# Kernel tuning notes

Hardware: AMD Instinct MI355X
Metric: run time of the kernel (lower is better)

## Reference

```python
import jax, jax.numpy as jnp
import numpy as np

C = 256; G = 16; GC = C // G; K = 3; P = K * K
N = 4; H = 64; W = 64
PAD = 1; OFFSET_SCALE = 1.0; LN_EPS = 1e-5


def setup_inputs() -> dict:
    key = jax.random.key(0)
    ks = jax.random.split(key, 8)
    s = 0.02
    return {
        "x": jax.random.normal(ks[0], (N, C, H, W), jnp.float32),
        "dw_w": jax.random.normal(ks[1], (C, 1, K, K), jnp.float32) * s,
        "dw_b": jnp.zeros((C,), jnp.float32),
        "ln_g": jnp.ones((C,), jnp.float32),
        "ln_b": jnp.zeros((C,), jnp.float32),
        "off_w": jax.random.normal(ks[2], (C, G * P * 2), jnp.float32) * s,
        "off_b": jnp.zeros((G * P * 2,), jnp.float32),
        "mask_w": jax.random.normal(ks[3], (C, G * P), jnp.float32) * s,
        "mask_b": jnp.zeros((G * P,), jnp.float32),
        "inp_w": jax.random.normal(ks[4], (C, C), jnp.float32) * s,
        "inp_b": jnp.zeros((C,), jnp.float32),
        "out_w": jax.random.normal(ks[5], (C, C), jnp.float32) * s,
        "out_b": jnp.zeros((C,), jnp.float32),
    }


def _dcnv3_nchw(x, dw_w, dw_b, ln_g, ln_b, off_w, off_b, mask_w, mask_b,
                inp_w, inp_b, out_w, out_b):
    # NCHW -> NHWC (wrapper permute)
    xn = jnp.transpose(x, (0, 2, 3, 1))                      # (N,H,W,C)
    x_proj = xn @ inp_w + inp_b                              # input_proj

    # offset/mask branch: depthwise conv (NCHW) -> LayerNorm (channels-last) -> GELU
    x1 = jax.lax.conv_general_dilated(
        x, dw_w, window_strides=(1, 1), padding=((PAD, PAD), (PAD, PAD)),
        dimension_numbers=("NCHW", "OIHW", "NCHW"), feature_group_count=C)
    x1 = jnp.transpose(x1, (0, 2, 3, 1)) + dw_b
    mu = x1.mean(-1, keepdims=True)
    var = ((x1 - mu) ** 2).mean(-1, keepdims=True)
    x1 = (x1 - mu) * jax.lax.rsqrt(var + LN_EPS) * ln_g + ln_b
    x1 = jax.nn.gelu(x1, approximate=False)

    offset = (x1 @ off_w + off_b).reshape(N, H, W, G, P, 2)  # (x,y) pairs
    mask = jax.nn.softmax((x1 @ mask_w + mask_b).reshape(N, H, W, G, P), axis=-1)

    # pad sampled feature map with zeros (F.pad before sampling)
    xp = jnp.pad(x_proj, ((0, 0), (PAD, PAD), (PAD, PAD), (0, 0)))
    Hin, Win = H + 2 * PAD, W + 2 * PAD
    xg = xp.reshape(N, Hin, Win, G, GC)

    # reference points, normalized by padded size
    ref_y = (jnp.arange(H, dtype=jnp.float32) + PAD + 0.5) / Hin
    ref_x = (jnp.arange(W, dtype=jnp.float32) + PAD + 0.5) / Win
    ref = jnp.stack([jnp.broadcast_to(ref_x[None, :], (H, W)),
                     jnp.broadcast_to(ref_y[:, None], (H, W))], -1)  # (H,W,2)

    # dilation grid: x varies in the outer loop (torch meshgrid 'ij')
    d = jnp.arange(K, dtype=jnp.float32) - (K - 1) // 2     # [-1,0,1]
    gx = jnp.repeat(d, K) / Win
    gy = jnp.tile(d, K) / Hin
    grid = jnp.stack([gx, gy], -1)                           # (P,2)

    norm = jnp.array([Win, Hin], jnp.float32)
    loc = (ref[None, :, :, None, None, :] + grid * OFFSET_SCALE
           + offset * OFFSET_SCALE / norm)                   # (N,H,W,G,P,2)

    # grid_sample bilinear, align_corners=False, zero padding
    px = loc[..., 0] * Win - 0.5
    py = loc[..., 1] * Hin - 0.5
    x0 = jnp.floor(px); y0 = jnp.floor(py)
    wx = px - x0; wy = py - y0
    x0i = x0.astype(jnp.int32); y0i = y0.astype(jnp.int32)

    n_idx = jnp.arange(N)[:, None, None, None, None]
    g_idx = jnp.arange(G)[None, None, None, :, None]

    def corner(iy, ix, w):
        valid = (iy >= 0) & (iy < Hin) & (ix >= 0) & (ix < Win)
        v = xg[n_idx, jnp.clip(iy, 0, Hin - 1), jnp.clip(ix, 0, Win - 1), g_idx]
        wgt = jnp.where(valid, w, 0.0) * mask                # fold mask into weights
        return jnp.einsum("nhwgp,nhwgpc->nhwgc", wgt, v)

    out = (corner(y0i, x0i, (1 - wy) * (1 - wx))
           + corner(y0i, x0i + 1, (1 - wy) * wx)
           + corner(y0i + 1, x0i, wy * (1 - wx))
           + corner(y0i + 1, x0i + 1, wy * wx))               # (N,H,W,G,GC)

    out = out.reshape(N, H, W, C) @ out_w + out_b            # output_proj
    return jnp.transpose(out, (0, 3, 1, 2))                  # NHWC -> NCHW


def reference(x, dw_w, dw_b, ln_g, ln_b, off_w, off_b, mask_w, mask_b,
              inp_w, inp_b, out_w, out_b):
    return _dcnv3_nchw(x, dw_w, dw_b, ln_g, ln_b, off_w, off_b,
                       mask_w, mask_b, inp_w, inp_b, out_w, out_b)
```

## Files before the change

### kernel.cpp

```cpp
#include <hip/hip_runtime.h>
#include <hip/hip_bf16.h>
#include <math.h>


using bf16x8 = __attribute__((ext_vector_type(8))) short;
using f32x4  = __attribute__((ext_vector_type(4))) float;

#define GLOBAL_AS __attribute__((address_space(1)))
#define LDS_AS    __attribute__((address_space(3)))

static __device__ inline void g2lds16(const void* g, void* l) {
  __builtin_amdgcn_global_load_lds((const GLOBAL_AS int*)g, (LDS_AS int*)l, 16, 0, 0);
}
static __device__ inline unsigned short f2bf(float v) {
  __hip_bfloat16 b = __float2bfloat16(v);
  return *reinterpret_cast<unsigned short*>(&b);
}
static __device__ inline float us2f(unsigned short u) {
  union { unsigned u; float f; } c; c.u = ((unsigned)u) << 16; return c.f;
}

__global__ __launch_bounds__(256) void prep_xt_k(
    const float* __restrict__ x,
    const float* __restrict__ inp_w, const float* __restrict__ off_w,
    const float* __restrict__ off_b, const float* __restrict__ mask_w,
    const float* __restrict__ mask_b, const float* __restrict__ out_w,
    __hip_bfloat16* __restrict__ BtI, __hip_bfloat16* __restrict__ BtOM,
    __hip_bfloat16* __restrict__ BtO, float* __restrict__ bOM,
    __hip_bfloat16* __restrict__ xT)
{
  __shared__ float tile[32][65];
  const int b = blockIdx.x, t = threadIdx.x;
  if (b < 1024) {
    if (b < 256) {
      int n = b;
      BtI[n * 256 + t] = __float2bfloat16(inp_w[t * 256 + n]);
    } else if (b < 768) {
      int n = b - 256;
      float v = 0.f;
      if (n < 288) v = off_w[t * 288 + n];
      else if (n < 432) v = mask_w[t * 144 + (n - 288)];
      BtOM[n * 256 + t] = __float2bfloat16(v);
      if (b == 256) {
        for (int idx = t; idx < 512; idx += 256) {
          float bv = (idx < 288) ? off_b[idx] : ((idx < 432) ? mask_b[idx - 288] : 0.f);
          bOM[idx] = bv;
        }
      }
    } else {
      int n = b - 768;
      BtO[n * 256 + t] = __float2bfloat16(out_w[t * 256 + n]);
    }
    return;
  }
  const int i = b - 1024;
  const int hw0 = (i & 63) * 64, c0 = ((i >> 6) & 7) * 32, n4 = i >> 9;
  #pragma unroll
  for (int r = 0; r < 8; ++r) {
    int idx = t + r * 256;
    int cl = idx >> 6, wl = idx & 63;
    tile[cl][wl] = x[(size_t)n4 * 1048576 + (size_t)(c0 + cl) * 4096 + hw0 + wl];
  }
  __syncthreads();
  #pragma unroll
  for (int r = 0; r < 2; ++r) {
    int idx = t + r * 256;
    int pixl = idx >> 3, cq = idx & 7;
    unsigned short b0 = f2bf(tile[cq * 4 + 0][pixl]);
    unsigned short b1 = f2bf(tile[cq * 4 + 1][pixl]);
    unsigned short b2 = f2bf(tile[cq * 4 + 2][pixl]);
    unsigned short b3 = f2bf(tile[cq * 4 + 3][pixl]);
    uint2 u;
    u.x = (unsigned)b0 | ((unsigned)b1 << 16);
    u.y = (unsigned)b2 | ((unsigned)b3 << 16);
    *(uint2*)&xT[((size_t)n4 * 4096 + hw0 + pixl) * 256 + c0 + cq * 4] = u;
  }
}

struct G64 {
  f32x4 acc[2][2];
  int lane, quad, lr, wm, wn;
};

static __device__ inline void g64_loop(
    G64& g, const __hip_bfloat16* __restrict__ A,
    const __hip_bfloat16* __restrict__ Bt, size_t m0, int n0,
    short* As, short* Bs, int t)
{
  #pragma unroll
  for (int i = 0; i < 2; ++i)
    #pragma unroll
    for (int j = 0; j < 2; ++j)
      g.acc[i][j] = (f32x4){0.f, 0.f, 0.f, 0.f};
  const int row = t >> 2, kq = t & 3;
  for (int kt = 0; kt < 256; kt += 32) {
    g2lds16(A + (m0 + row) * 256 + kt + kq * 8, (char*)As + t * 16);
    g2lds16(Bt + (size_t)(n0 + row) * 256 + kt + kq * 8, (char*)Bs + t * 16);
    __syncthreads();
    bf16x8 bfv[2];
    #pragma unroll
    for (int ni = 0; ni < 2; ++ni)
      bfv[ni] = *(const bf16x8*)&Bs[(g.wn * 32 + ni * 16 + g.lr) * 32 + g.quad * 8];
    #pragma unroll
    for (int mi = 0; mi < 2; ++mi) {
      bf16x8 af = *(const bf16x8*)&As[(g.wm * 32 + mi * 16 + g.lr) * 32 + g.quad * 8];
      #pragma unroll
      for (int ni = 0; ni < 2; ++ni)
        g.acc[mi][ni] = __builtin_amdgcn_mfma_f32_16x16x32_bf16(af, bfv[ni], g.acc[mi][ni], 0, 0, 0);
    }
    __syncthreads();
  }
}

__global__ __launch_bounds__(1024) void stage2_gi_k(
    const float* __restrict__ x,
    const __hip_bfloat16* __restrict__ xT,
    const float* __restrict__ dw_w, const float* __restrict__ dw_b,
    const float* __restrict__ ln_g, const float* __restrict__ ln_b,
    const __hip_bfloat16* __restrict__ BtOM, const float* __restrict__ bOM,
    __hip_bfloat16* __restrict__ om,
    const __hip_bfloat16* __restrict__ BtI, const float* __restrict__ inp_b,
    __hip_bfloat16* __restrict__ xpu)
{
  __shared__ __align__(16) char smem[62464];
  const int bid = blockIdx.x;

  if (bid >= 256) {
    const int sb = threadIdx.x >> 8;
    const int t = threadIdx.x & 255;
    const int tile = (bid - 256) * 4 + sb;
    const int n0 = (tile & 3) * 64;
    const size_t m0 = (size_t)(tile >> 2) * 64;
    short* As = (short*)(smem + sb * 8192);
    short* Bs = (short*)(smem + sb * 8192 + 4096);

    G64 g;
    g.lane = t & 63; g.quad = g.lane >> 4; g.lr = g.lane & 15;
    int wave = t >> 6;
    g.wm = wave >> 1; g.wn = wave & 1;
    g64_loop(g, xT, BtI, m0, n0, As, Bs, t);

    #pragma unroll
    for (int mi = 0; mi < 2; ++mi) {
      #pragma unroll
      for (int ni = 0; ni < 2; ++ni) {
        int col = n0 + g.wn * 32 + ni * 16 + g.lr;
        float bv = inp_b[col];
        #pragma unroll
        for (int reg = 0; reg < 4; ++reg) {
          size_t m = m0 + g.wm * 32 + mi * 16 + g.quad * 4 + reg;
          xpu[m * 256 + col] = __float2bfloat16(g.acc[mi][ni][reg] + bv);
        }
      }
    }
    return;
  }

  unsigned short* x1t = (unsigned short*)smem;
  float* psq  = (float*)(smem + 33792);
  float* murs = (float*)(smem + 41984);
  short* Bs   = (short*)(smem + 33792);

  const int blk = ((bid & 7) << 5) | (bid >> 3);
  const int n4 = blk >> 6, h = blk & 63;
  const int t = threadIdx.x;
  const int w = t & 63, q = t >> 6;

  const float* xb = x + (size_t)n4 * 1048576;
  const bool hm = (h > 0), hp = (h < 63);
  float av[16];
  float s1 = 0.f, s2 = 0.f;

  #pragma unroll 2
  for (int j = 0; j < 8; ++j) {
    #pragma unroll
    for (int u = 0; u < 2; ++u) {
      const int c = q * 16 + 2 * j + u;
      const float* xc = xb + (size_t)c * 4096 + h * 64 + w;
      float v0 = hm ? xc[-64] : 0.f;
      float v1 = xc[0];
      float v2 = hp ? xc[64] : 0.f;
      const float* wp = dw_w + c * 9;
      float a = dw_b[c];
      float vr0 = v0, vr1 = v1, vr2 = v2;
      #pragma unroll
      for (int dh = 0; dh < 3; ++dh) {
        float v = (dh == 0) ? vr0 : (dh == 1) ? vr1 : vr2;
        float vm = __shfl(v, w - 1, 64);
        float vp = __shfl(v, w + 1, 64);
        if (w == 0)  vm = 0.f;
        if (w == 63) vp = 0.f;
        a = fmaf(vm, wp[dh * 3 + 0], a);
        a = fmaf(v,  wp[dh * 3 + 1], a);
        a = fmaf(vp, wp[dh * 3 + 2], a);
      }
      s1 += a;
      s2 = fmaf(a, a, s2);
      av[2 * j + u] = a;
    }
  }

  psq[q * 64 + w] = s1;
  psq[1024 + q * 64 + w] = s2;
  __syncthreads();
  if (t < 64) {
    float a = 0.f, b = 0.f;
    #pragma unroll
    for (int j = 0; j < 16; ++j) { a += psq[j * 64 + t]; b += psq[1024 + j * 64 + t]; }
    float mu = a * (1.f / 256.f);
    murs[t] = mu;
    murs[64 + t] = rsqrtf(b * (1.f / 256.f) - mu * mu + 1e-5f);
  }
  __syncthreads();
  {
    float mu = murs[w], rs = murs[64 + w];
    #pragma unroll
    for (int j = 0; j < 8; ++j) {
      int c = q * 16 + 2 * j;
      float y0 = fmaf((av[2 * j] - mu) * rs, ln_g[c], ln_b[c]);
      float y1 = fmaf((av[2 * j + 1] - mu) * rs, ln_g[c + 1], ln_b[c + 1]);
      float g0 = 0.5f * y0 * (1.f + erff(y0 * 0.70710678f));
      float g1 = 0.5f * y1 * (1.f + erff(y1 * 0.70710678f));
      *(unsigned*)&x1t[w * 264 + c] = (unsigned)f2bf(g0) | ((unsigned)f2bf(g1) << 16);
    }
  }
  __syncthreads();

  const int wave = t >> 6, lane = t & 63;
  const int quad = lane >> 4, lr = lane & 15;
  const int wm = wave >> 2, wn = wave & 3;
  f32x4 acc[7];
  #pragma unroll
  for (int i = 0; i < 7; ++i) acc[i] = (f32x4){0.f, 0.f, 0.f, 0.f};

  for (int kt = 0; kt < 256; kt += 32) {
    __syncthreads();
    {
      int col = t >> 2, kq = t & 3;
      g2lds16(BtOM + (size_t)col * 256 + kt + kq * 8, (char*)Bs + t * 16);
      int jj = t + 1024;
      if (jj < 1792) {
        col = jj >> 2; kq = jj & 3;
        g2lds16(BtOM + (size_t)col * 256 + kt + kq * 8, (char*)Bs + jj * 16);
      }
    }
    __syncthreads();
    bf16x8 af = *(const bf16x8*)&x1t[(wm * 16 + lr) * 264 + kt + quad * 8];
    #pragma unroll
    for (int ni = 0; ni < 7; ++ni) {
      bf16x8 bf = *(const bf16x8*)&Bs[(wn * 112 + ni * 16 + lr) * 32 + quad * 8];
      acc[ni] = __builtin_amdgcn_mfma_f32_16x16x32_bf16(af, bf, acc[ni], 0, 0, 0);
    }
  }

  const size_t pix0 = (size_t)n4 * 4096 + (size_t)h * 64;
  #pragma unroll
  for (int ni = 0; ni < 7; ++ni) {
    int col = wn * 112 + ni * 16 + lr;
    if (col < 432) {
      float bv = bOM[col];
      #pragma unroll
      for (int reg = 0; reg < 4; ++reg) {
        int m = wm * 16 + quad * 4 + reg;
        om[(pix0 + m) * 448 + col] = __float2bfloat16(acc[ni][reg] + bv);
      }
    }
  }
}

__global__ __launch_bounds__(1024) void fused_so_k(
    const __hip_bfloat16* __restrict__ xpu, const __hip_bfloat16* __restrict__ om,
    const __hip_bfloat16* __restrict__ BtO, const float* __restrict__ out_b,
    float* __restrict__ out)
{
  __shared__ __align__(16) char smem[50176];
  unsigned short* st = (unsigned short*)smem;
  short* Bs = (short*)(smem + 33792);

  const int bid = blockIdx.x;
  const int swz = ((bid & 7) << 5) | (bid >> 3);
  const int pix0 = swz << 6;
  const int t = threadIdx.x;

  {
    const int pl = t >> 4, g = t & 15;
    const int pix = pix0 + pl;
    const int n4s = pix >> 12;
    const int hw = pix & 4095;
    const int h = hw >> 6, w = hw & 63;
    const unsigned short* omp = (const unsigned short*)om + (size_t)pix * 448;

    float mk[9];
    {
      float mx = -1e30f;
      #pragma unroll
      for (int p = 0; p < 9; ++p) { mk[p] = us2f(omp[288 + g * 9 + p]); mx = fmaxf(mx, mk[p]); }
      float se = 0.f;
      #pragma unroll
      for (int p = 0; p < 9; ++p) { mk[p] = __expf(mk[p] - mx); se += mk[p]; }
      float inv = 1.f / se;
      #pragma unroll
      for (int p = 0; p < 9; ++p) mk[p] *= inv;
    }

    const __hip_bfloat16* xpg = xpu + (g << 4);
    float ax[16];
    #pragma unroll
    for (int i = 0; i < 16; ++i) ax[i] = 0.f;

    auto corner = [&](int iy, int ix, float wt) {
      if ((unsigned)(iy - 1) >= 64u || (unsigned)(ix - 1) >= 64u) return;
      const __hip_bfloat16* src =
          xpg + ((size_t)((n4s << 12) + (iy - 1) * 64 + (ix - 1)) << 8);
      uint4 u0 = *(const uint4*)src;
      uint4 u1 = *(const uint4*)(src + 8);
      const unsigned uu[8] = {u0.x, u0.y, u0.z, u0.w, u1.x, u1.y, u1.z, u1.w};
      #pragma unroll
      for (int i = 0; i < 8; ++i) {
        float lo = us2f((unsigned short)(uu[i] & 0xffff));
        float hi = us2f((unsigned short)(uu[i] >> 16));
        ax[2 * i + 0] = fmaf(wt, lo, ax[2 * i + 0]);
        ax[2 * i + 1] = fmaf(wt, hi, ax[2 * i + 1]);
      }
    };

    #pragma unroll
    for (int p = 0; p < 9; ++p) {
      float ox = us2f(omp[g * 18 + 2 * p]), oy = us2f(omp[g * 18 + 2 * p + 1]);
      float px = (float)(w + p / 3) + ox;
      float py = (float)(h + p % 3) + oy;
      float xf = floorf(px), yf = floorf(py);
      float wx = px - xf, wy = py - yf;
      int ix = (int)xf, iy = (int)yf;
      float m = mk[p];
      corner(iy,     ix,     (1.f - wy) * (1.f - wx) * m);
      corner(iy,     ix + 1, (1.f - wy) * wx * m);
      corner(iy + 1, ix,     wy * (1.f - wx) * m);
      corner(iy + 1, ix + 1, wy * wx * m);
    }

    unsigned short ub[16];
    #pragma unroll
    for (int i = 0; i < 16; ++i) ub[i] = f2bf(ax[i]);
    uint4 u0, u1;
    u0.x = (unsigned)ub[0] | ((unsigned)ub[1] << 16);
    u0.y = (unsigned)ub[2] | ((unsigned)ub[3] << 16);
    u0.z = (unsigned)ub[4] | ((unsigned)ub[5] << 16);
    u0.w = (unsigned)ub[6] | ((unsigned)ub[7] << 16);
    u1.x = (unsigned)ub[8] | ((unsigned)ub[9] << 16);
    u1.y = (unsigned)ub[10] | ((unsigned)ub[11] << 16);
    u1.z = (unsigned)ub[12] | ((unsigned)ub[13] << 16);
    u1.w = (unsigned)ub[14] | ((unsigned)ub[15] << 16);
    *(uint4*)&st[pl * 264 + g * 16] = u0;
    *(uint4*)&st[pl * 264 + g * 16 + 8] = u1;
  }

  const int wave = t >> 6, lane = t & 63;
  const int quad = lane >> 4, lr = lane & 15;
  const int wm = wave >> 2, wn = wave & 3;
  f32x4 acc[4];
  #pragma unroll
  for (int i = 0; i < 4; ++i) acc[i] = (f32x4){0.f, 0.f, 0.f, 0.f};

  for (int kt = 0; kt < 256; kt += 32) {
    __syncthreads();
    {
      int col = t >> 2, kq = t & 3;
      g2lds16(BtO + (size_t)col * 256 + kt + kq * 8, (char*)Bs + t * 16);
    }
    __syncthreads();
    bf16x8 af = *(const bf16x8*)&st[(wm * 16 + lr) * 264 + kt + quad * 8];
    #pragma unroll
    for (int ni = 0; ni < 4; ++ni) {
      bf16x8 bf = *(const bf16x8*)&Bs[(wn * 64 + ni * 16 + lr) * 32 + quad * 8];
      acc[ni] = __builtin_amdgcn_mfma_f32_16x16x32_bf16(af, bf, acc[ni], 0, 0, 0);
    }
  }

  const int n4 = pix0 >> 12, hw0 = pix0 & 4095;
  #pragma unroll
  for (int ni = 0; ni < 4; ++ni) {
    int col = wn * 64 + ni * 16 + lr;
    float bv = out_b[col];
    float4 v;
    v.x = acc[ni][0] + bv; v.y = acc[ni][1] + bv;
    v.z = acc[ni][2] + bv; v.w = acc[ni][3] + bv;
    *(float4*)&out[(size_t)(n4 * 256 + col) * 4096 + hw0 + wm * 16 + quad * 4] = v;
  }
}

extern "C" void kernel_launch(void* const* d_in, const int* in_sizes, int n_in,
                              void* d_out, int out_size, void* d_ws, size_t ws_size,
                              hipStream_t stream) {
  const float* x      = (const float*)d_in[0];
  const float* dw_w   = (const float*)d_in[1];
  const float* dw_b   = (const float*)d_in[2];
  const float* ln_g   = (const float*)d_in[3];
  const float* ln_b   = (const float*)d_in[4];
  const float* off_w  = (const float*)d_in[5];
  const float* off_b  = (const float*)d_in[6];
  const float* mask_w = (const float*)d_in[7];
  const float* mask_b = (const float*)d_in[8];
  const float* inp_w  = (const float*)d_in[9];
  const float* inp_b  = (const float*)d_in[10];
  const float* out_w  = (const float*)d_in[11];
  const float* out_b  = (const float*)d_in[12];
  float* out = (float*)d_out;

  char* w0 = (char*)d_ws;
  __hip_bfloat16* xpu  = (__hip_bfloat16*)(w0);
  __hip_bfloat16* xT   = (__hip_bfloat16*)(w0 + 8388608);
  __hip_bfloat16* om   = (__hip_bfloat16*)(w0 + 16777216);
  __hip_bfloat16* BtI  = (__hip_bfloat16*)(w0 + 31457280);
  __hip_bfloat16* BtOM = (__hip_bfloat16*)(w0 + 31588352);
  __hip_bfloat16* BtO  = (__hip_bfloat16*)(w0 + 31850496);
  float*          bOM  = (float*)(w0 + 31981568);
  if (ws_size < 31983616) return;

  prep_xt_k<<<3072, 256, 0, stream>>>(x, inp_w, off_w, off_b, mask_w, mask_b,
                                      out_w, BtI, BtOM, BtO, bOM, xT);
  stage2_gi_k<<<512, 1024, 0, stream>>>(x, xT, dw_w, dw_b, ln_g, ln_b, BtOM, bOM,
                                        om, BtI, inp_b, xpu);
  fused_so_k<<<256, 1024, 0, stream>>>(xpu, om, BtO, out_b, out);
}
```

Before: 157.6 us.

## Fuse NCHW transpose into input-projection GEMM and halve sampling block size

Removes the separate xT transpose buffer. The input-projection blocks of stage2 now read the fp32 NCHW input directly, transpose it through LDS into a bf16 A-tile, and run a 64x256 MFMA GEMM against BtI, saving an 8 MB intermediate write and read. The fused sampling/output-projection kernel moves from 256 blocks of 1024 threads on 64 pixels to 512 blocks of 512 threads on 32 pixels, using less LDS per block. The cost is that the in-kernel transpose serializes eight chunk loads with barriers, and BtI is re-read by every strip block.

```diff
diff --git a/kernel.cpp b/kernel.cpp
--- a/kernel.cpp
+++ b/kernel.cpp
@@ -20,101 +20,37 @@
   union { unsigned u; float f; } c; c.u = ((unsigned)u) << 16; return c.f;
 }
 
-__global__ __launch_bounds__(256) void prep_xt_k(
-    const float* __restrict__ x,
+__global__ __launch_bounds__(256) void prep_w_k(
     const float* __restrict__ inp_w, const float* __restrict__ off_w,
     const float* __restrict__ off_b, const float* __restrict__ mask_w,
     const float* __restrict__ mask_b, const float* __restrict__ out_w,
     __hip_bfloat16* __restrict__ BtI, __hip_bfloat16* __restrict__ BtOM,
-    __hip_bfloat16* __restrict__ BtO, float* __restrict__ bOM,
-    __hip_bfloat16* __restrict__ xT)
+    __hip_bfloat16* __restrict__ BtO, float* __restrict__ bOM)
 {
-  __shared__ float tile[32][65];
   const int b = blockIdx.x, t = threadIdx.x;
-  if (b < 1024) {
-    if (b < 256) {
-      int n = b;
-      BtI[n * 256 + t] = __float2bfloat16(inp_w[t * 256 + n]);
-    } else if (b < 768) {
-      int n = b - 256;
-      float v = 0.f;
-      if (n < 288) v = off_w[t * 288 + n];
-      else if (n < 432) v = mask_w[t * 144 + (n - 288)];
-      BtOM[n * 256 + t] = __float2bfloat16(v);
-      if (b == 256) {
-        for (int idx = t; idx < 512; idx += 256) {
-          float bv = (idx < 288) ? off_b[idx] : ((idx < 432) ? mask_b[idx - 288] : 0.f);
-          bOM[idx] = bv;
-        }
-      }
-    } else {
-      int n = b - 768;
-      BtO[n * 256 + t] = __float2bfloat16(out_w[t * 256 + n]);
-    }
-    return;
-  }
-  const int i = b - 1024;
-  const int hw0 = (i & 63) * 64, c0 = ((i >> 6) & 7) * 32, n4 = i >> 9;
-  #pragma unroll
-  for (int r = 0; r < 8; ++r) {
-    int idx = t + r * 256;
-    int cl = idx >> 6, wl = idx & 63;
-    tile[cl][wl] = x[(size_t)n4 * 1048576 + (size_t)(c0 + cl) * 4096 + hw0 + wl];
-  }
-  __syncthreads();
-  #pragma unroll
-  for (int r = 0; r < 2; ++r) {
-    int idx = t + r * 256;
-    int pixl = idx >> 3, cq = idx & 7;
-    unsigned short b0 = f2bf(tile[cq * 4 + 0][pixl]);
-    unsigned short b1 = f2bf(tile[cq * 4 + 1][pixl]);
-    unsigned short b2 = f2bf(tile[cq * 4 + 2][pixl]);
-    unsigned short b3 = f2bf(tile[cq * 4 + 3][pixl]);
-    uint2 u;
-    u.x = (unsigned)b0 | ((unsigned)b1 << 16);
-    u.y = (unsigned)b2 | ((unsigned)b3 << 16);
-    *(uint2*)&xT[((size_t)n4 * 4096 + hw0 + pixl) * 256 + c0 + cq * 4] = u;
-  }
-}
-
-struct G64 {
-  f32x4 acc[2][2];
-  int lane, quad, lr, wm, wn;
-};
-
-static __device__ inline void g64_loop(
-    G64& g, const __hip_bfloat16* __restrict__ A,
-    const __hip_bfloat16* __restrict__ Bt, size_t m0, int n0,
-    short* As, short* Bs, int t)
-{
-  #pragma unroll
-  for (int i = 0; i < 2; ++i)
-    #pragma unroll
-    for (int j = 0; j < 2; ++j)
-      g.acc[i][j] = (f32x4){0.f, 0.f, 0.f, 0.f};
-  const int row = t >> 2, kq = t & 3;
-  for (int kt = 0; kt < 256; kt += 32) {
-    g2lds16(A + (m0 + row) * 256 + kt + kq * 8, (char*)As + t * 16);
-    g2lds16(Bt + (size_t)(n0 + row) * 256 + kt + kq * 8, (char*)Bs + t * 16);
-    __syncthreads();
-    bf16x8 bfv[2];
-    #pragma unroll
-    for (int ni = 0; ni < 2; ++ni)
-      bfv[ni] = *(const bf16x8*)&Bs[(g.wn * 32 + ni * 16 + g.lr) * 32 + g.quad * 8];
-    #pragma unroll
-    for (int mi = 0; mi < 2; ++mi) {
-      bf16x8 af = *(const bf16x8*)&As[(g.wm * 32 + mi * 16 + g.lr) * 32 + g.quad * 8];
-      #pragma unroll
-      for (int ni = 0; ni < 2; ++ni)
-        g.acc[mi][ni] = __builtin_amdgcn_mfma_f32_16x16x32_bf16(af, bfv[ni], g.acc[mi][ni], 0, 0, 0);
-    }
-    __syncthreads();
+  if (b < 256) {
+    int n = b;
+    BtI[n * 256 + t] = __float2bfloat16(inp_w[t * 256 + n]);
+  } else if (b < 768) {
+    int n = b - 256;
+    float v = 0.f;
+    if (n < 288) v = off_w[t * 288 + n];
+    else if (n < 432) v = mask_w[t * 144 + (n - 288)];
+    BtOM[n * 256 + t] = __float2bfloat16(v);
+    if (b == 256) {
+      for (int idx = t; idx < 512; idx += 256) {
+        float bv = (idx < 288) ? off_b[idx] : ((idx < 432) ? mask_b[idx - 288] : 0.f);
+        bOM[idx] = bv;
+      }
+    }
+  } else {
+    int n = b - 768;
+    BtO[n * 256 + t] = __float2bfloat16(out_w[t * 256 + n]);
   }
 }
 
 __global__ __launch_bounds__(1024) void stage2_gi_k(
     const float* __restrict__ x,
-    const __hip_bfloat16* __restrict__ xT,
     const float* __restrict__ dw_w, const float* __restrict__ dw_b,
     const float* __restrict__ ln_g, const float* __restrict__ ln_b,
     const __hip_bfloat16* __restrict__ BtOM, const float* __restrict__ bOM,
@@ -124,33 +60,67 @@
 {
   __shared__ __align__(16) char smem[62464];
   const int bid = blockIdx.x;
+  const int t = threadIdx.x;
 
   if (bid >= 256) {
-    const int sb = threadIdx.x >> 8;
-    const int t = threadIdx.x & 255;
-    const int tile = (bid - 256) * 4 + sb;
-    const int n0 = (tile & 3) * 64;
-    const size_t m0 = (size_t)(tile >> 2) * 64;
-    short* As = (short*)(smem + sb * 8192);
-    short* Bs = (short*)(smem + sb * 8192 + 4096);
-
-    G64 g;
-    g.lane = t & 63; g.quad = g.lane >> 4; g.lr = g.lane & 15;
-    int wave = t >> 6;
-    g.wm = wave >> 1; g.wn = wave & 1;
-    g64_loop(g, xT, BtI, m0, n0, As, Bs, t);
-
-    #pragma unroll
-    for (int mi = 0; mi < 2; ++mi) {
-      #pragma unroll
-      for (int ni = 0; ni < 2; ++ni) {
-        int col = n0 + g.wn * 32 + ni * 16 + g.lr;
-        float bv = inp_b[col];
-        #pragma unroll
-        for (int reg = 0; reg < 4; ++reg) {
-          size_t m = m0 + g.wm * 32 + mi * 16 + g.quad * 4 + reg;
-          xpu[m * 256 + col] = __float2bfloat16(g.acc[mi][ni][reg] + bv);
-        }
+    unsigned short* A = (unsigned short*)smem;
+    float* ftile = (float*)(smem + 33792);
+    short* Bs = (short*)(smem + 42112);
+
+    const int strip = bid - 256;
+    const int n4 = strip >> 6, hw0 = (strip & 63) * 64;
+    const float* xb = x + (size_t)n4 * 1048576 + hw0;
+
+    for (int ck = 0; ck < 8; ++ck) {
+      const int ch0 = ck * 32;
+      #pragma unroll
+      for (int r = 0; r < 2; ++r) {
+        int idx = t + r * 1024;
+        int cl = idx >> 6, wl = idx & 63;
+        ftile[cl * 65 + wl] = xb[(size_t)(ch0 + cl) * 4096 + wl];
+      }
+      __syncthreads();
+      {
+        int px = t >> 4, cq2 = t & 15;
+        unsigned short b0 = f2bf(ftile[(cq2 * 2) * 65 + px]);
+        unsigned short b1 = f2bf(ftile[(cq2 * 2 + 1) * 65 + px]);
+        *(unsigned*)&A[px * 264 + ch0 + cq2 * 2] =
+            (unsigned)b0 | ((unsigned)b1 << 16);
+      }
+      __syncthreads();
+    }
+
+    const int wave = t >> 6, lane = t & 63;
+    const int quad = lane >> 4, lr = lane & 15;
+    const int wm = wave >> 2, wn = wave & 3;
+    f32x4 acc[4];
+    #pragma unroll
+    for (int i = 0; i < 4; ++i) acc[i] = (f32x4){0.f, 0.f, 0.f, 0.f};
+
+    for (int kt = 0; kt < 256; kt += 32) {
+      __syncthreads();
+      {
+        int col = t >> 2, kq = t & 3;
+        g2lds16(BtI + (size_t)col * 256 + kt + kq * 8, (char*)Bs + t * 16);
+      }
+      __syncthreads();
+      bf16x8 af = *(const bf16x8*)&A[(wm * 16 + lr) * 264 + kt + quad * 8];
+      #pragma unroll
+      for (int ni = 0; ni < 4; ++ni) {
+        bf16x8 bf = *(const bf16x8*)&Bs[(wn * 64 + ni * 16 + lr) * 32 + quad * 8];
+        acc[ni] = __builtin_amdgcn_mfma_f32_16x16x32_bf16(af, bf, acc[ni], 0, 0, 0);
+      }
+    }
+
+    const size_t m0 = (size_t)strip * 64;
+    #pragma unroll
+    for (int ni = 0; ni < 4; ++ni) {
+      int col = wn * 64 + ni * 16 + lr;
+      float bv = inp_b[col];
+      #pragma unroll
+      for (int reg = 0; reg < 4; ++reg) {
+        size_t m = m0 + wm * 16 + quad * 4 + reg;
+        xpu[m * 256 + col] = __float2bfloat16(acc[ni][reg] + bv);
       }
     }
     return;
@@ -163,7 +133,6 @@
 
   const int blk = ((bid & 7) << 5) | (bid >> 3);
   const int n4 = blk >> 6, h = blk & 63;
-  const int t = threadIdx.x;
   const int w = t & 63, q = t >> 6;
 
   const float* xb = x + (size_t)n4 * 1048576;
@@ -182,10 +151,9 @@
       float v2 = hp ? xc[64] : 0.f;
       const float* wp = dw_w + c * 9;
       float a = dw_b[c];
-      float vr0 = v0, vr1 = v1, vr2 = v2;
       #pragma unroll
       for (int dh = 0; dh < 3; ++dh) {
-        float v = (dh == 0) ? vr0 : (dh == 1) ? vr1 : vr2;
+        float v = (dh == 0) ? v0 : (dh == 1) ? v1 : v2;
         float vm = __shfl(v, w - 1, 64);
         float vp = __shfl(v, w + 1, 64);
         if (w == 0)  vm = 0.f;
@@ -268,18 +236,18 @@
   }
 }
 
-__global__ __launch_bounds__(1024) void fused_so_k(
+__global__ __launch_bounds__(512) void fused_so_k(
     const __hip_bfloat16* __restrict__ xpu, const __hip_bfloat16* __restrict__ om,
     const __hip_bfloat16* __restrict__ BtO, const float* __restrict__ out_b,
     float* __restrict__ out)
 {
-  __shared__ __align__(16) char smem[50176];
+  __shared__ __align__(16) char smem[33792];
   unsigned short* st = (unsigned short*)smem;
-  short* Bs = (short*)(smem + 33792);
+  short* Bs = (short*)(smem + 16896);
 
   const int bid = blockIdx.x;
-  const int swz = ((bid & 7) << 5) | (bid >> 3);
-  const int pix0 = swz << 6;
+  const int swz = ((bid & 7) << 6) | (bid >> 3);
+  const int pix0 = swz << 5;
   const int t = threadIdx.x;
 
   {
@@ -365,8 +333,12 @@
   for (int kt = 0; kt < 256; kt += 32) {
     __syncthreads();
     {
-      int col = t >> 2, kq = t & 3;
-      g2lds16(BtO + (size_t)col * 256 + kt + kq * 8, (char*)Bs + t * 16);
+      #pragma unroll
+      for (int r = 0; r < 2; ++r) {
+        int j = t + r * 512;
+        int col = j >> 2, kq = j & 3;
+        g2lds16(BtO + (size_t)col * 256 + kt + kq * 8, (char*)Bs + j * 16);
+      }
     }
     __syncthreads();
     bf16x8 af = *(const bf16x8*)&st[(wm * 16 + lr) * 264 + kt + quad * 8];
@@ -409,17 +381,16 @@
 
   char* w0 = (char*)d_ws;
   __hip_bfloat16* xpu  = (__hip_bfloat16*)(w0);
-  __hip_bfloat16* xT   = (__hip_bfloat16*)(w0 + 8388608);
-  __hip_bfloat16* om   = (__hip_bfloat16*)(w0 + 16777216);
-  __hip_bfloat16* BtI  = (__hip_bfloat16*)(w0 + 31457280);
-  __hip_bfloat16* BtOM = (__hip_bfloat16*)(w0 + 31588352);
-  __hip_bfloat16* BtO  = (__hip_bfloat16*)(w0 + 31850496);
-  float*          bOM  = (float*)(w0 + 31981568);
-  if (ws_size < 31983616) return;
-
-  prep_xt_k<<<3072, 256, 0, stream>>>(x, inp_w, off_w, off_b, mask_w, mask_b,
-                                      out_w, BtI, BtOM, BtO, bOM, xT);
-  stage2_gi_k<<<512, 1024, 0, stream>>>(x, xT, dw_w, dw_b, ln_g, ln_b, BtOM, bOM,
+  __hip_bfloat16* om   = (__hip_bfloat16*)(w0 + 8388608);
+  __hip_bfloat16* BtI  = (__hip_bfloat16*)(w0 + 23068672);
+  __hip_bfloat16* BtOM = (__hip_bfloat16*)(w0 + 23199744);
+  __hip_bfloat16* BtO  = (__hip_bfloat16*)(w0 + 23461888);
+  float*          bOM  = (float*)(w0 + 23592960);
+  if (ws_size < 23595008) return;
+
+  prep_w_k<<<1024, 256, 0, stream>>>(inp_w, off_w, off_b, mask_w, mask_b,
+                                     out_w, BtI, BtOM, BtO, bOM);
+  stage2_gi_k<<<512, 1024, 0, stream>>>(x, dw_w, dw_b, ln_g, ln_b, BtOM, bOM,
                                         om, BtI, inp_b, xpu);
-  fused_so_k<<<256, 1024, 0, stream>>>(xpu, om, BtO, out_b, out);
-}
+  fused_so_k<<<512, 512, 0, stream>>>(xpu, om, BtO, out_b, out);
+}
```

Measured after the change: 156.8 us. No clear change (-0.5%).
